# Kernel tuning notes

Measured on AMD Instinct MI355X. Metric: run time of the kernel, lower is better.

The kernel has to match this reference:

```python
import jax, jax.numpy as jnp
import numpy as np

N = 100000   # total nodes
E = 600000   # total edges
G = 2048     # graphs in batch
DIN = 9      # input node feature dim
D = 128      # hidden == output dim
L = 5        # GIN layers
BN_EPS = 1e-5
LN_EPS = 1e-5


def setup_inputs() -> dict:
    key = jax.random.key(0)
    ks = jax.random.split(key, 24)
    s = 0.05
    x = jax.random.normal(ks[0], (N, DIN), jnp.float32)
    edge_index = jax.random.randint(ks[1], (2, E), 0, N, dtype=jnp.int32)
    batch = jnp.sort(jax.random.randint(ks[2], (N,), 0, G, dtype=jnp.int32))
    return {
        "x": x,
        "edge_index": edge_index,
        "batch": batch,
        # node embedding
        "node_emb_W": jax.random.normal(ks[3], (DIN, D), jnp.float32) * s,
        "node_emb_b": jnp.zeros((D,), jnp.float32),
        # GIN layer MLPs, stacked over layers: Linear(D,2D) -> ReLU -> Linear(2D,D)
        "W1s": jax.random.normal(ks[4], (L, D, 2 * D), jnp.float32) * s,
        "b1s": jnp.zeros((L, 2 * D), jnp.float32),
        "W2s": jax.random.normal(ks[5], (L, 2 * D, D), jnp.float32) * s,
        "b2s": jnp.zeros((L, D), jnp.float32),
        # BatchNorm affine params per layer
        "bn_g": jnp.ones((L, D), jnp.float32),
        "bn_b": jnp.zeros((L, D), jnp.float32),
        # virtual node
        "vn_emb": jax.random.normal(ks[6], (1, D), jnp.float32),
        "vn_W1": jax.random.normal(ks[7], (D, D), jnp.float32) * s,
        "vn_b1": jnp.zeros((D,), jnp.float32),
        "vn_W2": jax.random.normal(ks[8], (D, D), jnp.float32) * s,
        "vn_b2": jnp.zeros((D,), jnp.float32),
        # graph MLP: Linear -> LayerNorm -> ReLU -> Linear
        "gm_W1": jax.random.normal(ks[9], (D, D), jnp.float32) * s,
        "gm_b1": jnp.zeros((D,), jnp.float32),
        "ln_g": jnp.ones((D,), jnp.float32),
        "ln_b": jnp.zeros((D,), jnp.float32),
        "gm_W2": jax.random.normal(ks[10], (D, D), jnp.float32) * s,
        "gm_b2": jnp.zeros((D,), jnp.float32),
    }


def _mean_pool(h, batch):
    # segment mean over graphs: [N, D] -> [G, D]
    s = jax.ops.segment_sum(h, batch, num_segments=G)
    cnt = jax.ops.segment_sum(jnp.ones((h.shape[0], 1), h.dtype), batch, num_segments=G)
    return s / jnp.maximum(cnt, 1.0)


def _batchnorm(m, g, b):
    mu = jnp.mean(m, axis=0)
    var = jnp.mean(jnp.square(m - mu), axis=0)  # biased var (torch train-mode norm)
    return (m - mu) * jax.lax.rsqrt(var + BN_EPS) * g + b


def reference(x, edge_index, batch, node_emb_W, node_emb_b, W1s, b1s, W2s, b2s,
              bn_g, bn_b, vn_emb, vn_W1, vn_b1, vn_W2, vn_b2,
              gm_W1, gm_b1, ln_g, ln_b, gm_W2, gm_b2):
    src, dst = edge_index[0], edge_index[1]
    h = x @ node_emb_W + node_emb_b                       # [N, D]
    vn = jnp.tile(vn_emb, (G, 1))                         # [G, D]
    for i in range(L):
        h_prev = h
        # GINConv (eps=0): mlp(h + sum_{j->i} h_j) via gather/scatter-add
        agg = jax.ops.segment_sum(h[src], dst, num_segments=N)
        m = h + agg
        m = jax.nn.relu(m @ W1s[i] + b1s[i]) @ W2s[i] + b2s[i]
        h = jax.nn.relu(_batchnorm(m, bn_g[i], bn_b[i]))
        # (dropout is identity in eval mode)
        if i > 0:
            h = h + h_prev
        # virtual node: pool -> MLP -> broadcast back
        temp = _mean_pool(h, batch)                       # [G, D]
        vn = vn + (jax.nn.relu(temp @ vn_W1 + vn_b1) @ vn_W2 + vn_b2)
        h = h + vn[batch]
    node_features = h                                     # output_projection = Identity
    gf = _mean_pool(node_features, batch)                 # [G, D]
    gf = gf @ gm_W1 + gm_b1
    mu = jnp.mean(gf, axis=-1, keepdims=True)
    var = jnp.mean(jnp.square(gf - mu), axis=-1, keepdims=True)
    gf = (gf - mu) * jax.lax.rsqrt(var + LN_EPS) * ln_g + ln_b
    gf = jax.nn.relu(gf)
    graph_features = gf @ gm_W2 + gm_b2
    return node_features, graph_features
```

## Files before the change

kernel.cpp:

```cpp
#include <hip/hip_runtime.h>
#include <stdint.h>

#define NNODES 100000
#define NEDGES 600000
#define NGRAPH 2048
#define DD 128
#define NLAYER 5
#define NPAD 100096
#define SCAN_NB 391
#define NSTAT 32

typedef __attribute__((ext_vector_type(8))) __bf16 bf16x8;
typedef __attribute__((ext_vector_type(4))) float f32x4;
typedef __attribute__((ext_vector_type(8))) ushort u16x8;

__device__ __forceinline__ ushort f2b(float f) {
    union { float f; uint32_t u; } v; v.f = f;
    uint32_t r = v.u + 0x7FFFu + ((v.u >> 16) & 1u);
    return (ushort)(r >> 16);
}

__device__ __forceinline__ float b2f(ushort u) {
    union { uint32_t u; float f; } v; v.u = ((uint32_t)u) << 16; return v.f;
}

__device__ __forceinline__ void gload_lds16(const void* g, void* l) {
    __builtin_amdgcn_global_load_lds(
        (const __attribute__((address_space(1))) void*)g,
        (__attribute__((address_space(3))) void*)l, 16, 0, 0);
}

__global__ void prep_w_kernel(const float* __restrict__ W1s, const float* __restrict__ W2s,
                              ushort* __restrict__ w1t, ushort* __restrict__ w2t) {
    int idx = blockIdx.x * 256 + threadIdx.x;
    const int per = 128 * 256;
    if (idx < NLAYER * per) {
        int i = idx / per, rem = idx % per;
        int n = rem >> 7, k = rem & 127;
        w1t[idx] = f2b(W1s[(size_t)i * per + k * 256 + n]);
    } else if (idx < 2 * NLAYER * per) {
        int j = idx - NLAYER * per;
        int i = j / per, rem = j % per;
        int n = rem >> 8, k = rem & 255;
        w2t[j] = f2b(W2s[(size_t)i * per + k * 128 + n]);
    }
}

__global__ void node_embed_kernel(const float* __restrict__ x, const float* __restrict__ W,
                                  const float* __restrict__ b, ushort* __restrict__ hb,
                                  const float* __restrict__ vne, float* __restrict__ vn) {
    int idx = blockIdx.x * 256 + threadIdx.x;
    if (idx < NNODES * 128) {
        int n = idx >> 7, d = idx & 127;
        float v = b[d];
#pragma unroll
        for (int k = 0; k < 9; ++k) v += x[n * 9 + k] * W[k * 128 + d];
        hb[(size_t)n * 128 + d] = f2b(v);
    } else if (idx < NNODES * 128 + NGRAPH * 128) {
        int r = idx - NNODES * 128;
        vn[r] = vne[r & 127];
    }
}


__global__ void deg_kernel(const int* __restrict__ dst, int* __restrict__ deg) {
    int e = blockIdx.x * 256 + threadIdx.x;
    if (e < NEDGES) atomicAdd(&deg[dst[e]], 1);
}

__global__ void scan_part_kernel(const int* __restrict__ deg, int* __restrict__ partials) {
    int i = blockIdx.x * 256 + threadIdx.x;
    int lane = threadIdx.x & 63, w = threadIdx.x >> 6;
    int v = (i < NNODES) ? deg[i] : 0;
#pragma unroll
    for (int o = 1; o < 64; o <<= 1) v += __shfl_xor(v, o);
    __shared__ int ws[4];
    if (lane == 0) ws[w] = v;
    __syncthreads();
    if (threadIdx.x == 0) partials[blockIdx.x] = ws[0] + ws[1] + ws[2] + ws[3];
}

__global__ __launch_bounds__(512)
void scan_top_kernel(int* __restrict__ partials) {
    __shared__ int s[512];
    int t = threadIdx.x;
    int v = (t < SCAN_NB) ? partials[t] : 0;
    s[t] = v;
    __syncthreads();
#pragma unroll
    for (int o = 1; o < 512; o <<= 1) {
        int n = (t >= o) ? s[t - o] : 0;
        __syncthreads();
        s[t] += n;
        __syncthreads();
    }
    if (t < SCAN_NB) partials[t] = s[t] - v;
}

__global__ void scan_blocks_kernel(const int* __restrict__ deg, const int* __restrict__ partials,
                                   int* __restrict__ rs, int* __restrict__ cursor) {
    int i = blockIdx.x * 256 + threadIdx.x;
    int lane = threadIdx.x & 63, w = threadIdx.x >> 6;
    int v = (i < NNODES) ? deg[i] : 0;
    int x = v;
#pragma unroll
    for (int o = 1; o < 64; o <<= 1) {
        int n = __shfl_up(x, o);
        if (lane >= o) x += n;
    }
    __shared__ int ws[4];
    if (lane == 63) ws[w] = x;
    __syncthreads();
    if (threadIdx.x == 0) {
        int a = 0;
#pragma unroll
        for (int k = 0; k < 4; ++k) { int t = ws[k]; ws[k] = a; a += t; }
    }
    __syncthreads();
    int excl = (x - v) + ws[w] + partials[blockIdx.x];
    if (i < NNODES) { rs[i] = excl; cursor[i] = excl; }
    if (i == 0) rs[NNODES] = NEDGES;
}

__global__ void csr_scatter_kernel(const int* __restrict__ src, const int* __restrict__ dst,
                                   int* __restrict__ cursor, int* __restrict__ csrc) {
    int e = blockIdx.x * 256 + threadIdx.x;
    if (e < NEDGES) {
        int p = atomicAdd(&cursor[dst[e]], 1);
        csrc[p] = src[e];
    }
}

__device__ __forceinline__ int lbound(const int* __restrict__ b, int key) {
    int lo = 0, hi = NNODES;
    while (lo < hi) { int m = (lo + hi) >> 1; if (b[m] < key) lo = m + 1; else hi = m; }
    return lo;
}

__global__ void gstart_kernel(const int* __restrict__ batch, int* __restrict__ gstart,
                              float* __restrict__ inv) {
    int g = blockIdx.x * 256 + threadIdx.x;
    if (g <= NGRAPH)
        gstart[g] = (g == NGRAPH) ? NNODES : lbound(batch, g);
    if (g < NGRAPH) {
        int c = lbound(batch, g + 1) - lbound(batch, g);
        inv[g] = 1.f / (float)(c > 0 ? c : 1);
    }
}


__global__ __launch_bounds__(256)
void gin_agg_kernel(const ushort* __restrict__ hb, const int* __restrict__ rs,
                    const int* __restrict__ csrc, ushort* __restrict__ xb,
                    float* __restrict__ stats) {
    if (blockIdx.x < NSTAT) stats[blockIdx.x * 256 + threadIdx.x] = 0.f;
    int slot = threadIdx.x >> 4;
    int j = threadIdx.x & 15;
    int node = blockIdx.x * 16 + slot;
    if (node >= NNODES) return;
    int s = rs[node], e = rs[node + 1];
    u16x8 v0 = *(const u16x8*)(hb + (size_t)node * 128 + j * 8);
    float a[8], b[8];
#pragma unroll
    for (int t = 0; t < 8; ++t) { a[t] = b2f(v0[t]); b[t] = 0.f; }
    int k = s;
    for (; k + 3 < e; k += 4) {
        int s0 = csrc[k], s1 = csrc[k + 1], s2 = csrc[k + 2], s3 = csrc[k + 3];
        u16x8 va = *(const u16x8*)(hb + (size_t)s0 * 128 + j * 8);
        u16x8 vb = *(const u16x8*)(hb + (size_t)s1 * 128 + j * 8);
        u16x8 vc = *(const u16x8*)(hb + (size_t)s2 * 128 + j * 8);
        u16x8 vd = *(const u16x8*)(hb + (size_t)s3 * 128 + j * 8);
#pragma unroll
        for (int t = 0; t < 8; ++t) {
            a[t] += b2f(va[t]) + b2f(vc[t]);
            b[t] += b2f(vb[t]) + b2f(vd[t]);
        }
    }
    for (; k < e; ++k) {
        int s0 = csrc[k];
        u16x8 va = *(const u16x8*)(hb + (size_t)s0 * 128 + j * 8);
#pragma unroll
        for (int t = 0; t < 8; ++t) a[t] += b2f(va[t]);
    }
    u16x8 o;
#pragma unroll
    for (int t = 0; t < 8; ++t) o[t] = f2b(a[t] + b[t]);
    *(u16x8*)(xb + (size_t)node * 128 + j * 8) = o;
}

#define MLP_TILES 4
#define MLP_GRID 391
__global__ __launch_bounds__(256, 2)
void fused_mlp_kernel(const ushort* __restrict__ A, const ushort* __restrict__ W1,
                      const float* __restrict__ b1, const ushort* __restrict__ W2,
                      const float* __restrict__ b2, ushort* __restrict__ out_b,
                      float* __restrict__ stats) {
    __shared__ __align__(16) ushort lA[8192];
    __shared__ __align__(16) ushort mid[16384];
    const int tid = threadIdx.x;
    const int lane = tid & 63, w = tid >> 6;
    const int q = lane >> 4, l16 = lane & 15;
    float* sbase = stats + (blockIdx.x & (NSTAT - 1)) * 256;

    bf16x8 w1f[4][4], w2f[8][2];
#pragma unroll
    for (int ks = 0; ks < 4; ++ks)
#pragma unroll
        for (int ni = 0; ni < 4; ++ni)
            w1f[ks][ni] = *(const bf16x8*)(W1 + (size_t)(w * 64 + ni * 16 + l16) * 128 + ks * 32 + q * 8);
#pragma unroll
    for (int ks = 0; ks < 8; ++ks)
#pragma unroll
        for (int ni = 0; ni < 2; ++ni)
            w2f[ks][ni] = *(const bf16x8*)(W2 + (size_t)(w * 32 + ni * 16 + l16) * 256 + ks * 32 + q * 8);

    {
        int rb = blockIdx.x * (64 * MLP_TILES);
#pragma unroll
        for (int p = 0; p < 4; ++p)
            gload_lds16(A + (size_t)(rb + lane) * 128 + p * 32 + w * 8,
                        &lA[(size_t)(p * 256 + w * 64 + lane) * 8]);
    }

    for (int tt = 0; tt < MLP_TILES; ++tt) {
        const int rb = blockIdx.x * (64 * MLP_TILES) + tt * 64;
        __syncthreads();

        f32x4 acc1[4][4] = {};
#pragma unroll
        for (int ks = 0; ks < 4; ++ks) {
            bf16x8 af[4];
#pragma unroll
            for (int mi = 0; mi < 4; ++mi)
                af[mi] = *(const bf16x8*)&lA[ks * 2048 + q * 512 + (mi * 16 + l16) * 8];
#pragma unroll
            for (int mi = 0; mi < 4; ++mi)
#pragma unroll
                for (int ni = 0; ni < 4; ++ni)
                    acc1[mi][ni] = __builtin_amdgcn_mfma_f32_16x16x32_bf16(af[mi], w1f[ks][ni], acc1[mi][ni], 0, 0, 0);
        }

#pragma unroll
        for (int ni = 0; ni < 4; ++ni) {
            int col = w * 64 + ni * 16 + l16;
            float bs = b1[col];
            int g2 = col >> 3, jj = col & 7;
#pragma unroll
            for (int mi = 0; mi < 4; ++mi) {
                int rowb = mi * 16 + q * 4;
#pragma unroll
                for (int r = 0; r < 4; ++r) {
                    float v = acc1[mi][ni][r] + bs;
                    v = v > 0.f ? v : 0.f;
                    mid[g2 * 512 + (rowb + r) * 8 + jj] = f2b(v);
                }
            }
        }
        __syncthreads();

        if (tt + 1 < MLP_TILES) {
            int rb2 = rb + 64;
#pragma unroll
            for (int p = 0; p < 4; ++p)
                gload_lds16(A + (size_t)(rb2 + lane) * 128 + p * 32 + w * 8,
                            &lA[(size_t)(p * 256 + w * 64 + lane) * 8]);
        }

        f32x4 acc2[4][2] = {};
#pragma unroll
        for (int ks = 0; ks < 8; ++ks) {
            bf16x8 af[4];
#pragma unroll
            for (int mi = 0; mi < 4; ++mi)
                af[mi] = *(const bf16x8*)&mid[(ks * 4 + q) * 512 + (mi * 16 + l16) * 8];
#pragma unroll
            for (int mi = 0; mi < 4; ++mi)
#pragma unroll
                for (int ni = 0; ni < 2; ++ni)
                    acc2[mi][ni] = __builtin_amdgcn_mfma_f32_16x16x32_bf16(af[mi], w2f[ks][ni], acc2[mi][ni], 0, 0, 0);
        }

#pragma unroll
        for (int ni = 0; ni < 2; ++ni) {
            int col = w * 32 + ni * 16 + l16;
            float bs = b2[col];
            float s = 0.f, sq = 0.f;
#pragma unroll
            for (int mi = 0; mi < 4; ++mi) {
                int row = rb + mi * 16 + q * 4;
#pragma unroll
                for (int r = 0; r < 4; ++r) {
                    float v = acc2[mi][ni][r] + bs;
                    out_b[(size_t)(row + r) * 128 + col] = f2b(v);
                    if (row + r < NNODES) { s += v; sq += v * v; }
                }
            }
            s  += __shfl_xor(s, 16);  s  += __shfl_xor(s, 32);
            sq += __shfl_xor(sq, 16); sq += __shfl_xor(sq, 32);
            if (lane < 16) {
                atomicAdd(&sbase[col], s);
                atomicAdd(&sbase[128 + col], sq);
            }
        }
    }
}

template<int FINAL>
__global__ __launch_bounds__(256)
void tail_kernel(const ushort* __restrict__ m, ushort* __restrict__ hb,
                 const float* __restrict__ stats,
                 const float* __restrict__ bng, const float* __restrict__ bnb,
                 const int* __restrict__ gstart, const float* __restrict__ inv,
                 const float* __restrict__ W1, const float* __restrict__ b1,
                 const float* __restrict__ W2, const float* __restrict__ b2,
                 float* __restrict__ vn, float* __restrict__ outN,
                 float* __restrict__ gf, int resid) {
    __shared__ float sC[128], sS[128];
    __shared__ float red[16][128];
    __shared__ float t[128], t1[128], vns[128];
    int g = blockIdx.x, tid = threadIdx.x;
    if (tid < 128) {
        int d = tid;
        float sum = 0.f, sq = 0.f;
#pragma unroll
        for (int c = 0; c < NSTAT; ++c) {
            sum += stats[c * 256 + d];
            sq  += stats[c * 256 + 128 + d];
        }
        float mu = sum * (1.f / NNODES);
        float var = sq * (1.f / NNODES) - mu * mu;
        var = var < 0.f ? 0.f : var;
        float sc = bng[d] * rsqrtf(var + 1e-5f);
        sC[d] = sc;
        sS[d] = bnb[d] - mu * sc;
    }
    __syncthreads();
    int j = tid & 15, rg = tid >> 4;
    float sc8[8], sh8[8], acc[8];
#pragma unroll
    for (int k = 0; k < 8; ++k) { sc8[k] = sC[j * 8 + k]; sh8[k] = sS[j * 8 + k]; acc[k] = 0.f; }
    int s = gstart[g], e = gstart[g + 1];

    for (int r = s + rg; r < e; r += 16) {
        u16x8 mv = *(const u16x8*)(m + (size_t)r * 128 + j * 8);
        float v[8];
#pragma unroll
        for (int k = 0; k < 8; ++k) v[k] = fmaxf(b2f(mv[k]) * sc8[k] + sh8[k], 0.f);
        if (resid) {
            u16x8 hv = *(const u16x8*)(hb + (size_t)r * 128 + j * 8);
#pragma unroll
            for (int k = 0; k < 8; ++k) v[k] += b2f(hv[k]);
        }
#pragma unroll
        for (int k = 0; k < 8; ++k) acc[k] += v[k];
    }
#pragma unroll
    for (int k = 0; k < 8; ++k) red[rg][j * 8 + k] = acc[k];
    __syncthreads();
    if (tid < 128) {
        int d = tid;
        float tot = 0.f;
#pragma unroll
        for (int r2 = 0; r2 < 16; ++r2) tot += red[r2][d];
        t[d] = tot * inv[g];
    }
    __syncthreads();
    if (tid < 128) {
        int d = tid;
        float a = b1[d];
        for (int k = 0; k < 128; ++k) a += t[k] * W1[k * 128 + d];
        t1[d] = fmaxf(a, 0.f);
    }
    __syncthreads();
    if (tid < 128) {
        int d = tid;
        float o = b2[d];
        for (int k = 0; k < 128; ++k) o += t1[k] * W2[k * 128 + d];
        float vnew = vn[(size_t)g * 128 + d] + o;
        vn[(size_t)g * 128 + d] = vnew;
        vns[d] = vnew;
        if (FINAL) gf[(size_t)g * 128 + d] = (e > s) ? (t[d] + vnew) : 0.f;
    }
    __syncthreads();

    float vg[8];
#pragma unroll
    for (int k = 0; k < 8; ++k) vg[k] = vns[j * 8 + k];

    for (int r = s + rg; r < e; r += 16) {
        u16x8 mv = *(const u16x8*)(m + (size_t)r * 128 + j * 8);
        float v[8];
#pragma unroll
        for (int k = 0; k < 8; ++k) v[k] = fmaxf(b2f(mv[k]) * sc8[k] + sh8[k], 0.f);
        if (resid) {
            u16x8 hv = *(const u16x8*)(hb + (size_t)r * 128 + j * 8);
#pragma unroll
            for (int k = 0; k < 8; ++k) v[k] += b2f(hv[k]);
        }
#pragma unroll
        for (int k = 0; k < 8; ++k) v[k] += vg[k];
        if (FINAL) {
            float4* op = (float4*)(outN + (size_t)r * 128 + j * 8);
            op[0] = make_float4(v[0], v[1], v[2], v[3]);
            op[1] = make_float4(v[4], v[5], v[6], v[7]);
        } else {
            u16x8 o;
#pragma unroll
            for (int k = 0; k < 8; ++k) o[k] = f2b(v[k]);
            *(u16x8*)(hb + (size_t)r * 128 + j * 8) = o;
        }
    }
}

__global__ __launch_bounds__(128)
void graph_mlp_kernel(const float* __restrict__ gf,
                      const float* __restrict__ W1, const float* __restrict__ b1,
                      const float* __restrict__ lng, const float* __restrict__ lnb,
                      const float* __restrict__ W2, const float* __restrict__ b2,
                      float* __restrict__ out) {
    __shared__ float t[128], t1[128], lred[2];
    int g = blockIdx.x, d = threadIdx.x;
    int lane = d & 63, w = d >> 6;
    t[d] = gf[(size_t)g * 128 + d];
    __syncthreads();
    float a = b1[d];
    for (int k = 0; k < 128; ++k) a += t[k] * W1[k * 128 + d];
    float ssum = a;
#pragma unroll
    for (int o = 1; o < 64; o <<= 1) ssum += __shfl_xor(ssum, o);
    if (lane == 0) lred[w] = ssum;
    __syncthreads();
    float mu = (lred[0] + lred[1]) * (1.f / 128.f);
    float dv = a - mu;
    float qq = dv * dv;
#pragma unroll
    for (int o = 1; o < 64; o <<= 1) qq += __shfl_xor(qq, o);
    __syncthreads();
    if (lane == 0) lred[w] = qq;
    __syncthreads();
    float var = (lred[0] + lred[1]) * (1.f / 128.f);
    float v = dv * rsqrtf(var + 1e-5f) * lng[d] + lnb[d];
    v = fmaxf(v, 0.f);
    t1[d] = v;
    __syncthreads();
    float o2 = b2[d];
    for (int k = 0; k < 128; ++k) o2 += t1[k] * W2[k * 128 + d];
    out[g * 128 + d] = o2;
}

extern "C" void kernel_launch(void* const* d_in, const int* in_sizes, int n_in,
                              void* d_out, int out_size, void* d_ws, size_t ws_size,
                              hipStream_t stream) {
    const float* x    = (const float*)d_in[0];
    const int*   edge = (const int*)d_in[1];
    const int*   src  = edge;
    const int*   dst  = edge + NEDGES;
    const int*   batch = (const int*)d_in[2];
    const float* nW   = (const float*)d_in[3];
    const float* nb   = (const float*)d_in[4];
    const float* W1s  = (const float*)d_in[5];
    const float* b1s  = (const float*)d_in[6];
    const float* W2s  = (const float*)d_in[7];
    const float* b2s  = (const float*)d_in[8];
    const float* bng  = (const float*)d_in[9];
    const float* bnb  = (const float*)d_in[10];
    const float* vne  = (const float*)d_in[11];
    const float* vW1  = (const float*)d_in[12];
    const float* vb1  = (const float*)d_in[13];
    const float* vW2  = (const float*)d_in[14];
    const float* vb2  = (const float*)d_in[15];
    const float* gW1  = (const float*)d_in[16];
    const float* gb1  = (const float*)d_in[17];
    const float* lng  = (const float*)d_in[18];
    const float* lnb  = (const float*)d_in[19];
    const float* gW2  = (const float*)d_in[20];
    const float* gb2  = (const float*)d_in[21];

    char* ws = (char*)d_ws;
    auto alloc = [&](size_t bytes) { char* p = ws; ws += (bytes + 255) & ~(size_t)255; return p; };
    float*  stats = (float*)alloc((size_t)NSTAT * 256 * 4);
    ushort* hb    = (ushort*)alloc((size_t)NPAD * 128 * 2);
    ushort* mbuf  = (ushort*)alloc((size_t)NPAD * 128 * 2);
    ushort* xb    = (ushort*)alloc((size_t)NPAD * 128 * 2);
    float*  vn    = (float*)alloc((size_t)NGRAPH * 128 * 4);
    float*  gf    = (float*)alloc((size_t)NGRAPH * 128 * 4);
    ushort* w1t   = (ushort*)alloc((size_t)NLAYER * 256 * 128 * 2);
    ushort* w2t   = (ushort*)alloc((size_t)NLAYER * 128 * 256 * 2);
    float*  inv   = (float*)alloc((size_t)NGRAPH * 4);
    int*    gstart= (int*)alloc((size_t)(NGRAPH + 1) * 4);
    int*    deg   = (int*)alloc((size_t)NNODES * 4);
    int*    rs    = (int*)alloc((size_t)(NNODES + 1) * 4);
    int*    cursor= (int*)alloc((size_t)NNODES * 4);
    int*    csrc  = (int*)alloc((size_t)NEDGES * 4);
    int*    partials = (int*)alloc((size_t)SCAN_NB * 4);

    float* outN = (float*)d_out;
    float* outG = outN + (size_t)NNODES * 128;

    hipMemsetAsync(stats, 0, (size_t)NSTAT * 256 * 4, stream);
    hipMemsetAsync(deg, 0, (size_t)NNODES * 4, stream);

    deg_kernel<<<(NEDGES + 255) / 256, 256, 0, stream>>>(dst, deg);
    scan_part_kernel<<<SCAN_NB, 256, 0, stream>>>(deg, partials);
    scan_top_kernel<<<1, 512, 0, stream>>>(partials);
    scan_blocks_kernel<<<SCAN_NB, 256, 0, stream>>>(deg, partials, rs, cursor);
    csr_scatter_kernel<<<(NEDGES + 255) / 256, 256, 0, stream>>>(src, dst, cursor, csrc);
    gstart_kernel<<<(NGRAPH + 256) / 256, 256, 0, stream>>>(batch, gstart, inv);

    prep_w_kernel<<<(2 * NLAYER * 128 * 256 + 255) / 256, 256, 0, stream>>>(W1s, W2s, w1t, w2t);
    node_embed_kernel<<<((NNODES + NGRAPH) * 128 + 255) / 256, 256, 0, stream>>>(
        x, nW, nb, hb, vne, vn);

    for (int i = 0; i < NLAYER; ++i) {
        gin_agg_kernel<<<(NNODES + 15) / 16, 256, 0, stream>>>(hb, rs, csrc, xb, stats);
        fused_mlp_kernel<<<MLP_GRID, 256, 0, stream>>>(
            xb, w1t + (size_t)i * 256 * 128, b1s + i * 256,
            w2t + (size_t)i * 128 * 256, b2s + i * 128, mbuf, stats);
        if (i < NLAYER - 1)
            tail_kernel<0><<<NGRAPH, 256, 0, stream>>>(
                mbuf, hb, stats, bng + i * 128, bnb + i * 128, gstart, inv,
                vW1, vb1, vW2, vb2, vn, nullptr, nullptr, i > 0 ? 1 : 0);
        else
            tail_kernel<1><<<NGRAPH, 256, 0, stream>>>(
                mbuf, hb, stats, bng + i * 128, bnb + i * 128, gstart, inv,
                vW1, vb1, vW2, vb2, vn, outN, gf, 1);
    }
    graph_mlp_kernel<<<NGRAPH, 128, 0, stream>>>(gf, gW1, gb1, lng, lnb, gW2, gb2, outG);
}
```

Before: 576.1 us.

## Fuse GIN neighbor aggregation into the MLP kernel, removing the intermediate buffer

The separate gather/aggregation kernel is folded into the fused MLP kernel: each block now sums neighbor rows for its 64-node tile straight into LDS before running the MFMAs. This drops the xb intermediate write/read and one launch per layer. Stats zeroing moves into the same kernel, using double-buffered stats so the next layer's buffer can be cleared safely. W2 fragments are now loaded from global memory inside the k-loop instead of being kept in registers, and the async prefetch of the next A tile is gone. The risk is lower parallelism for the gather, since only 391 blocks of 256 threads handle it with 4 threads per node, so latency is less well hidden than with the old 6250-block kernel.

```diff
diff --git a/kernel.cpp b/kernel.cpp
--- a/kernel.cpp
+++ b/kernel.cpp
@@ -22,12 +22,6 @@
 
 __device__ __forceinline__ float b2f(ushort u) {
     union { uint32_t u; float f; } v; v.u = ((uint32_t)u) << 16; return v.f;
-}
-
-__device__ __forceinline__ void gload_lds16(const void* g, void* l) {
-    __builtin_amdgcn_global_load_lds(
-        (const __attribute__((address_space(1))) void*)g,
-        (__attribute__((address_space(3))) void*)l, 16, 0, 0);
 }
 
 __global__ void prep_w_kernel(const float* __restrict__ W1s, const float* __restrict__ W2s,
@@ -148,53 +142,15 @@
     }
 }
 
-
-__global__ __launch_bounds__(256)
-void gin_agg_kernel(const ushort* __restrict__ hb, const int* __restrict__ rs,
-                    const int* __restrict__ csrc, ushort* __restrict__ xb,
-                    float* __restrict__ stats) {
-    if (blockIdx.x < NSTAT) stats[blockIdx.x * 256 + threadIdx.x] = 0.f;
-    int slot = threadIdx.x >> 4;
-    int j = threadIdx.x & 15;
-    int node = blockIdx.x * 16 + slot;
-    if (node >= NNODES) return;
-    int s = rs[node], e = rs[node + 1];
-    u16x8 v0 = *(const u16x8*)(hb + (size_t)node * 128 + j * 8);
-    float a[8], b[8];
-#pragma unroll
-    for (int t = 0; t < 8; ++t) { a[t] = b2f(v0[t]); b[t] = 0.f; }
-    int k = s;
-    for (; k + 3 < e; k += 4) {
-        int s0 = csrc[k], s1 = csrc[k + 1], s2 = csrc[k + 2], s3 = csrc[k + 3];
-        u16x8 va = *(const u16x8*)(hb + (size_t)s0 * 128 + j * 8);
-        u16x8 vb = *(const u16x8*)(hb + (size_t)s1 * 128 + j * 8);
-        u16x8 vc = *(const u16x8*)(hb + (size_t)s2 * 128 + j * 8);
-        u16x8 vd = *(const u16x8*)(hb + (size_t)s3 * 128 + j * 8);
-#pragma unroll
-        for (int t = 0; t < 8; ++t) {
-            a[t] += b2f(va[t]) + b2f(vc[t]);
-            b[t] += b2f(vb[t]) + b2f(vd[t]);
-        }
-    }
-    for (; k < e; ++k) {
-        int s0 = csrc[k];
-        u16x8 va = *(const u16x8*)(hb + (size_t)s0 * 128 + j * 8);
-#pragma unroll
-        for (int t = 0; t < 8; ++t) a[t] += b2f(va[t]);
-    }
-    u16x8 o;
-#pragma unroll
-    for (int t = 0; t < 8; ++t) o[t] = f2b(a[t] + b[t]);
-    *(u16x8*)(xb + (size_t)node * 128 + j * 8) = o;
-}
-
 #define MLP_TILES 4
 #define MLP_GRID 391
 __global__ __launch_bounds__(256, 2)
-void fused_mlp_kernel(const ushort* __restrict__ A, const ushort* __restrict__ W1,
-                      const float* __restrict__ b1, const ushort* __restrict__ W2,
-                      const float* __restrict__ b2, ushort* __restrict__ out_b,
-                      float* __restrict__ stats) {
+void gin_mlp_kernel(const ushort* __restrict__ hb, const int* __restrict__ rs,
+                    const int* __restrict__ csrc,
+                    const ushort* __restrict__ W1, const float* __restrict__ b1,
+                    const ushort* __restrict__ W2, const float* __restrict__ b2,
+                    ushort* __restrict__ out_b, float* __restrict__ stats,
+                    float* __restrict__ statsZero) {
     __shared__ __align__(16) ushort lA[8192];
     __shared__ __align__(16) ushort mid[16384];
     const int tid = threadIdx.x;
@@ -202,28 +158,77 @@
     const int q = lane >> 4, l16 = lane & 15;
     float* sbase = stats + (blockIdx.x & (NSTAT - 1)) * 256;
 
-    bf16x8 w1f[4][4], w2f[8][2];
+    if (blockIdx.x < NSTAT) statsZero[blockIdx.x * 256 + tid] = 0.f;
+
+    bf16x8 w1f[4][4];
 #pragma unroll
     for (int ks = 0; ks < 4; ++ks)
 #pragma unroll
         for (int ni = 0; ni < 4; ++ni)
             w1f[ks][ni] = *(const bf16x8*)(W1 + (size_t)(w * 64 + ni * 16 + l16) * 128 + ks * 32 + q * 8);
-#pragma unroll
-    for (int ks = 0; ks < 8; ++ks)
-#pragma unroll
-        for (int ni = 0; ni < 2; ++ni)
-            w2f[ks][ni] = *(const bf16x8*)(W2 + (size_t)(w * 32 + ni * 16 + l16) * 256 + ks * 32 + q * 8);
-
-    {
-        int rb = blockIdx.x * (64 * MLP_TILES);
-#pragma unroll
-        for (int p = 0; p < 4; ++p)
-            gload_lds16(A + (size_t)(rb + lane) * 128 + p * 32 + w * 8,
-                        &lA[(size_t)(p * 256 + w * 64 + lane) * 8]);
-    }
+
+    const int row = tid >> 2, l4 = tid & 3;
 
     for (int tt = 0; tt < MLP_TILES; ++tt) {
         const int rb = blockIdx.x * (64 * MLP_TILES) + tt * 64;
+
+        {
+            int node = rb + row;
+            float acc[32];
+            if (node < NNODES) {
+                const ushort* hrow = hb + (size_t)node * 128 + l4 * 32;
+                u16x8 h0 = *(const u16x8*)(hrow);
+                u16x8 h1 = *(const u16x8*)(hrow + 8);
+                u16x8 h2 = *(const u16x8*)(hrow + 16);
+                u16x8 h3 = *(const u16x8*)(hrow + 24);
+#pragma unroll
+                for (int k = 0; k < 8; ++k) {
+                    acc[k] = b2f(h0[k]);      acc[8 + k]  = b2f(h1[k]);
+                    acc[16 + k] = b2f(h2[k]); acc[24 + k] = b2f(h3[k]);
+                }
+                int s = rs[node], e = rs[node + 1];
+                int k = s;
+                for (; k + 1 < e; k += 2) {
+                    const ushort* p0 = hb + (size_t)csrc[k] * 128 + l4 * 32;
+                    const ushort* p1 = hb + (size_t)csrc[k + 1] * 128 + l4 * 32;
+                    u16x8 a0 = *(const u16x8*)(p0);      u16x8 a1 = *(const u16x8*)(p0 + 8);
+                    u16x8 a2 = *(const u16x8*)(p0 + 16); u16x8 a3 = *(const u16x8*)(p0 + 24);
+                    u16x8 c0 = *(const u16x8*)(p1);      u16x8 c1 = *(const u16x8*)(p1 + 8);
+                    u16x8 c2 = *(const u16x8*)(p1 + 16); u16x8 c3 = *(const u16x8*)(p1 + 24);
+#pragma unroll
+                    for (int m = 0; m < 8; ++m) {
+                        acc[m]      += b2f(a0[m]) + b2f(c0[m]);
+                        acc[8 + m]  += b2f(a1[m]) + b2f(c1[m]);
+                        acc[16 + m] += b2f(a2[m]) + b2f(c2[m]);
+                        acc[24 + m] += b2f(a3[m]) + b2f(c3[m]);
+                    }
+                }
+                if (k < e) {
+                    const ushort* p0 = hb + (size_t)csrc[k] * 128 + l4 * 32;
+                    u16x8 a0 = *(const u16x8*)(p0);      u16x8 a1 = *(const u16x8*)(p0 + 8);
+                    u16x8 a2 = *(const u16x8*)(p0 + 16); u16x8 a3 = *(const u16x8*)(p0 + 24);
+#pragma unroll
+                    for (int m = 0; m < 8; ++m) {
+                        acc[m]      += b2f(a0[m]);
+                        acc[8 + m]  += b2f(a1[m]);
+                        acc[16 + m] += b2f(a2[m]);
+                        acc[24 + m] += b2f(a3[m]);
+                    }
+                }
+            } else {
+#pragma unroll
+                for (int m = 0; m < 32; ++m) acc[m] = 0.f;
+            }
+#pragma unroll
+            for (int c = 0; c < 4; ++c) {
+                int j = l4 * 4 + c;
+                int ks = j >> 2, qq = j & 3;
+                u16x8 o;
+#pragma unroll
+                for (int m = 0; m < 8; ++m) o[m] = f2b(acc[c * 8 + m]);
+                *(u16x8*)&lA[ks * 2048 + qq * 512 + row * 8] = o;
+            }
+        }
         __syncthreads();
 
         f32x4 acc1[4][4] = {};
@@ -258,26 +263,21 @@
         }
         __syncthreads();
 
-        if (tt + 1 < MLP_TILES) {
-            int rb2 = rb + 64;
-#pragma unroll
-            for (int p = 0; p < 4; ++p)
-                gload_lds16(A + (size_t)(rb2 + lane) * 128 + p * 32 + w * 8,
-                            &lA[(size_t)(p * 256 + w * 64 + lane) * 8]);
-        }
-
         f32x4 acc2[4][2] = {};
 #pragma unroll
         for (int ks = 0; ks < 8; ++ks) {
-            bf16x8 af[4];
+            bf16x8 af[4], bw[2];
 #pragma unroll
             for (int mi = 0; mi < 4; ++mi)
                 af[mi] = *(const bf16x8*)&mid[(ks * 4 + q) * 512 + (mi * 16 + l16) * 8];
 #pragma unroll
+            for (int ni = 0; ni < 2; ++ni)
+                bw[ni] = *(const bf16x8*)(W2 + (size_t)(w * 32 + ni * 16 + l16) * 256 + ks * 32 + q * 8);
+#pragma unroll
             for (int mi = 0; mi < 4; ++mi)
 #pragma unroll
                 for (int ni = 0; ni < 2; ++ni)
-                    acc2[mi][ni] = __builtin_amdgcn_mfma_f32_16x16x32_bf16(af[mi], w2f[ks][ni], acc2[mi][ni], 0, 0, 0);
+                    acc2[mi][ni] = __builtin_amdgcn_mfma_f32_16x16x32_bf16(af[mi], bw[ni], acc2[mi][ni], 0, 0, 0);
         }
 
 #pragma unroll
@@ -287,12 +287,12 @@
             float s = 0.f, sq = 0.f;
 #pragma unroll
             for (int mi = 0; mi < 4; ++mi) {
-                int row = rb + mi * 16 + q * 4;
+                int rr = rb + mi * 16 + q * 4;
 #pragma unroll
                 for (int r = 0; r < 4; ++r) {
                     float v = acc2[mi][ni][r] + bs;
-                    out_b[(size_t)(row + r) * 128 + col] = f2b(v);
-                    if (row + r < NNODES) { s += v; sq += v * v; }
+                    out_b[(size_t)(rr + r) * 128 + col] = f2b(v);
+                    if (rr + r < NNODES) { s += v; sq += v * v; }
                 }
             }
             s  += __shfl_xor(s, 16);  s  += __shfl_xor(s, 32);
@@ -302,6 +302,7 @@
                 atomicAdd(&sbase[128 + col], sq);
             }
         }
+        __syncthreads();
     }
 }
 
@@ -478,10 +479,9 @@
 
     char* ws = (char*)d_ws;
     auto alloc = [&](size_t bytes) { char* p = ws; ws += (bytes + 255) & ~(size_t)255; return p; };
-    float*  stats = (float*)alloc((size_t)NSTAT * 256 * 4);
+    float*  stats = (float*)alloc((size_t)2 * NSTAT * 256 * 4);
     ushort* hb    = (ushort*)alloc((size_t)NPAD * 128 * 2);
     ushort* mbuf  = (ushort*)alloc((size_t)NPAD * 128 * 2);
-    ushort* xb    = (ushort*)alloc((size_t)NPAD * 128 * 2);
     float*  vn    = (float*)alloc((size_t)NGRAPH * 128 * 4);
     float*  gf    = (float*)alloc((size_t)NGRAPH * 128 * 4);
     ushort* w1t   = (ushort*)alloc((size_t)NLAYER * 256 * 128 * 2);
@@ -497,7 +497,7 @@
     float* outN = (float*)d_out;
     float* outG = outN + (size_t)NNODES * 128;
 
-    hipMemsetAsync(stats, 0, (size_t)NSTAT * 256 * 4, stream);
+    hipMemsetAsync(stats, 0, (size_t)2 * NSTAT * 256 * 4, stream);
     hipMemsetAsync(deg, 0, (size_t)NNODES * 4, stream);
 
     deg_kernel<<<(NEDGES + 255) / 256, 256, 0, stream>>>(dst, deg);
@@ -512,17 +512,20 @@
         x, nW, nb, hb, vne, vn);
 
     for (int i = 0; i < NLAYER; ++i) {
-        gin_agg_kernel<<<(NNODES + 15) / 16, 256, 0, stream>>>(hb, rs, csrc, xb, stats);
-        fused_mlp_kernel<<<MLP_GRID, 256, 0, stream>>>(
-            xb, w1t + (size_t)i * 256 * 128, b1s + i * 256,
-            w2t + (size_t)i * 128 * 256, b2s + i * 128, mbuf, stats);
+        float* statsCur  = stats + (size_t)(i & 1) * NSTAT * 256;
+        float* statsNext = stats + (size_t)((i + 1) & 1) * NSTAT * 256;
+        gin_mlp_kernel<<<MLP_GRID, 256, 0, stream>>>(
+            hb, rs, csrc,
+            w1t + (size_t)i * 256 * 128, b1s + i * 256,
+            w2t + (size_t)i * 128 * 256, b2s + i * 128,
+            mbuf, statsCur, statsNext);
         if (i < NLAYER - 1)
             tail_kernel<0><<<NGRAPH, 256, 0, stream>>>(
-                mbuf, hb, stats, bng + i * 128, bnb + i * 128, gstart, inv,
+                mbuf, hb, statsCur, bng + i * 128, bnb + i * 128, gstart, inv,
                 vW1, vb1, vW2, vb2, vn, nullptr, nullptr, i > 0 ? 1 : 0);
         else
             tail_kernel<1><<<NGRAPH, 256, 0, stream>>>(
-                mbuf, hb, stats, bng + i * 128, bnb + i * 128, gstart, inv,
+                mbuf, hb, statsCur, bng + i * 128, bnb + i * 128, gstart, inv,
                 vW1, vb1, vW2, vb2, vn, outN, gf, 1);
     }
     graph_mlp_kernel<<<NGRAPH, 128, 0, stream>>>(gf, gW1, gb1, lng, lnb, gW2, gb2, outG);
```

Measured after the change: 573.4 us (median of 2 runs). Within noise of the previous version (-0.5%).
